# Optimization experiments

Hardware: AMD Instinct MI355X
Metric: run time of the kernel (lower is better)

Reference implementation:

```python
import jax, jax.numpy as jnp
import numpy as np
import math

B, L, H, E, D = 4, 2048, 8, 64, 64
EPS = 1e-6

def _adjust(x):
    # signed power-law (sqrt) then L2-normalize over feature dim
    y = jnp.sign(x) * jnp.sqrt(jnp.abs(x) + EPS)
    return y / (jnp.linalg.norm(y, axis=-1, keepdims=True) + EPS)

def setup_inputs() -> dict:
    key = jax.random.key(0)
    kq, kk, kv, ka = jax.random.split(key, 4)
    queries = jax.random.normal(kq, (B, L, H, E), dtype=jnp.float32)
    keys = jax.random.normal(kk, (B, L, H, E), dtype=jnp.float32)
    values = jax.random.normal(kv, (B, L, H, D), dtype=jnp.float32)
    # TriangularCausalMask: True above the diagonal => masked
    attn_mask = jnp.triu(jnp.ones((1, 1, L, L), dtype=bool), k=1)
    alpha = jax.random.normal(ka, (1,), dtype=jnp.float32) * 0.01
    return {"queries": queries, "keys": keys, "values": values,
            "attn_mask": attn_mask, "alpha": alpha}

def reference(queries, keys, values, attn_mask, alpha):
    Bq, Lq, Hq, Eq = queries.shape
    scale = 1.0 / math.sqrt(Eq)
    # Closed form of torch.autograd.functional.jacobian of
    # sum(einsum('blhe,bshe->bhls', q, k)):
    #   d/dq[b,l,h,e] = sum_s k[b,s,h,e]   (independent of l)
    #   d/dk[b,s,h,e] = sum_l q[b,l,h,e]   (independent of s)
    k_sum = jnp.sum(keys, axis=1, keepdims=True)      # [B,1,H,E]
    q_sum = jnp.sum(queries, axis=1, keepdims=True)   # [B,1,H,E]
    q_adj = _adjust(queries + alpha * k_sum)
    k_adj = _adjust(keys + alpha * q_sum)
    scores = jnp.einsum('blhe,bshe->bhls', q_adj, k_adj)  # [B,H,L,S]
    scores = jnp.where(attn_mask, -jnp.inf, scores)
    A = jax.nn.softmax(scale * scores, axis=-1)  # dropout inactive (eval)
    V = jnp.einsum('bhls,bshd->blhd', A, values)
    return V
```

## Files before the change

### kernel.cpp

```cpp
#include <hip/hip_runtime.h>
#include <hip/hip_bf16.h>
#include <math.h>

#define NB 4
#define NL 2048
#define NH 8
#define NE 64
#define ND 64
#define EPSF 1e-6f
#define CEXP 0.180336881f

typedef __attribute__((ext_vector_type(8))) short bf16x8;
typedef __attribute__((ext_vector_type(4))) float f32x4;

__global__ void sums_kernel(const float* __restrict__ q, const float* __restrict__ k,
                            float* __restrict__ qsum, float* __restrict__ ksum) {
  int bh = blockIdx.x;
  int lp = blockIdx.y;
  int e = threadIdx.x & 63, sub = threadIdx.x >> 6;
  int b = bh >> 3, h = bh & 7;
  size_t base = (((size_t)b * NL) * NH + h) * NE + e;
  const float* qp = q + base;
  const float* kp = k + base;
  float sq = 0.f, sk = 0.f;
#pragma unroll
  for (int i = 0; i < 16; ++i) {
    int l = lp * 64 + i * 4 + sub;
    size_t off = (size_t)l * NH * NE;
    sq += qp[off];
    sk += kp[off];
  }
  __shared__ float s1[256], s2[256];
  s1[threadIdx.x] = sq; s2[threadIdx.x] = sk;
  __syncthreads();
  if (sub == 0) {
    sq = s1[e] + s1[e + 64] + s1[e + 128] + s1[e + 192];
    sk = s2[e] + s2[e + 64] + s2[e + 128] + s2[e + 192];
    atomicAdd(&qsum[bh * NE + e], sq);
    atomicAdd(&ksum[bh * NE + e], sk);
  }
}

__global__ void adjust_kernel(const float* __restrict__ q, const float* __restrict__ k,
                              const float* __restrict__ qsum, const float* __restrict__ ksum,
                              const float* __restrict__ alpha,
                              __hip_bfloat16* __restrict__ qadj, __hip_bfloat16* __restrict__ kadj) {
  int wid = (int)((blockIdx.x * 256 + threadIdx.x) >> 6);
  int lane = threadIdx.x & 63;
  int h = wid & 7;
  int l = (wid >> 3) & (NL - 1);
  int b = wid >> 14;
  float al = alpha[0];
  size_t ioff = (((size_t)b * NL + l) * NH + h) * NE + lane;
  int bh = b * NH + h;
  float xq = q[ioff] + al * ksum[bh * NE + lane];
  float xk = k[ioff] + al * qsum[bh * NE + lane];
  float yq = (xq > 0.f) ? sqrtf(xq + EPSF) : ((xq < 0.f) ? -sqrtf(-xq + EPSF) : 0.f);
  float yk = (xk > 0.f) ? sqrtf(xk + EPSF) : ((xk < 0.f) ? -sqrtf(-xk + EPSF) : 0.f);
  float nq = yq * yq, nk = yk * yk;
#pragma unroll
  for (int m = 1; m < 64; m <<= 1) {
    nq += __shfl_xor(nq, m, 64);
    nk += __shfl_xor(nk, m, 64);
  }
  float rq = yq / (sqrtf(nq) + EPSF);
  float rk = yk / (sqrtf(nk) + EPSF);
  size_t ooff = ((size_t)bh * NL + l) * NE + lane;
  qadj[ooff] = __float2bfloat16(rq);
  kadj[ooff] = __float2bfloat16(rk);
}

__global__ void vtrans_kernel(const float* __restrict__ v, __hip_bfloat16* __restrict__ vt) {
  __shared__ __hip_bfloat16 tile[64][68];
  int s0 = blockIdx.x * 64;
  int bh = blockIdx.y;
  int b = bh >> 3, h = bh & 7;
  int t = threadIdx.x;
  {
    int sl = t >> 2, dg = t & 3;
    const float* src = v + (((size_t)b * NL + s0 + sl) * NH + h) * ND + dg * 16;
#pragma unroll
    for (int i = 0; i < 4; ++i) {
      float4 f = *(const float4*)(src + i * 4);
      tile[sl][dg * 16 + i * 4 + 0] = __float2bfloat16(f.x);
      tile[sl][dg * 16 + i * 4 + 1] = __float2bfloat16(f.y);
      tile[sl][dg * 16 + i * 4 + 2] = __float2bfloat16(f.z);
      tile[sl][dg * 16 + i * 4 + 3] = __float2bfloat16(f.w);
    }
  }
  __syncthreads();
  {
    int d = t >> 2, sg = t & 3;
    __align__(16) __hip_bfloat16 tmp[16];
#pragma unroll
    for (int i = 0; i < 16; ++i) tmp[i] = tile[sg * 16 + i][d];
    __hip_bfloat16* dst = vt + ((size_t)bh * ND + d) * NL + s0 + sg * 16;
    *(bf16x8*)(dst) = *(const bf16x8*)&tmp[0];
    *(bf16x8*)(dst + 8) = *(const bf16x8*)&tmp[8];
  }
}

__global__ __launch_bounds__(512) void attn_kernel(const __hip_bfloat16* __restrict__ qadj,
                                                   const __hip_bfloat16* __restrict__ kadj,
                                                   const __hip_bfloat16* __restrict__ vt,
                                                   float* __restrict__ out) {
  __shared__ __align__(16) char lds[49152];
  int bh = blockIdx.x;
  int pairid = blockIdx.y;
  int b = bh >> 3, h = bh & 7;
  int wave = threadIdx.x >> 6, lane = threadIdx.x & 63;
  int qr = lane & 15, eg = lane >> 4;
  char* ldsP = lds + 32768 + wave * 2048;
  const char* kgb = (const char*)(kadj + (size_t)bh * NL * NE);
  const char* vgb = (const char*)(vt + (size_t)bh * ND * NL);
  const char* qgb = (const char*)(qadj + (size_t)bh * NL * NE);

  auto STAGE = [&](int bufsel, int s0) {
    char* dstbase = lds + bufsel * 16384;
    if (wave < 4) {
#pragma unroll
      for (int c = 0; c < 2; ++c) {
        int T = wave * 2048 + c * 1024 + lane * 16;
        int S = T ^ (((T >> 7) & 7) << 4);
        __builtin_amdgcn_global_load_lds(
            (const __attribute__((address_space(1))) unsigned int*)(kgb + (size_t)s0 * 128 + S),
            (__attribute__((address_space(3))) unsigned int*)(dstbase + wave * 2048 + c * 1024),
            16, 0, 0);
      }
    } else {
      int w = wave - 4;
#pragma unroll
      for (int c = 0; c < 2; ++c) {
        int T = w * 2048 + c * 1024 + lane * 16;
        int S = T ^ (((T >> 7) & 7) << 4);
        int d = S >> 7, cc = S & 127;
        __builtin_amdgcn_global_load_lds(
            (const __attribute__((address_space(1))) unsigned int*)(vgb + ((size_t)d * NL + s0) * 2 + cc),
            (__attribute__((address_space(3))) unsigned int*)(dstbase + 8192 + w * 2048 + c * 1024),
            16, 0, 0);
      }
    }
  };

#pragma unroll 1
  for (int half = 0; half < 2; ++half) {
    int tile = (half == 0) ? pairid : (15 - pairid);
    int t0 = tile * 128;
    int nck = (t0 >> 6) + 2;
    int qw0 = t0 + wave * 16;

    bf16x8 qf0 = *(const bf16x8*)(qgb + ((size_t)(qw0 + qr) * NE + eg * 8) * 2);
    bf16x8 qf1 = *(const bf16x8*)(qgb + ((size_t)(qw0 + qr) * NE + 32 + eg * 8) * 2);

    f32x4 acc[4];
    float srun[4];
#pragma unroll
    for (int dc = 0; dc < 4; ++dc) acc[dc] = (f32x4){0.f, 0.f, 0.f, 0.f};
#pragma unroll
    for (int vv = 0; vv < 4; ++vv) srun[vv] = 0.f;

    STAGE(0, 0);
    asm volatile("s_waitcnt vmcnt(0)" ::: "memory");
    __builtin_amdgcn_sched_barrier(0);
    __builtin_amdgcn_s_barrier();

    int cur = 0;
#pragma unroll 1
    for (int ck = 0; ck < nck; ++ck) {
      int s0 = ck * 64;
      if (ck + 1 < nck) STAGE(cur ^ 1, s0 + 64);
      char* ldsK = lds + cur * 16384;
      char* ldsV = ldsK + 8192;

      float p[4][4];
#pragma unroll
      for (int st = 0; st < 4; ++st) {
        f32x4 a = (f32x4){0.f, 0.f, 0.f, 0.f};
        int row = st * 16 + qr;
        int swz = (row & 7) << 4;
        bf16x8 k0 = *(const bf16x8*)(ldsK + ((row * 128 + eg * 16) ^ swz));
        bf16x8 k1 = *(const bf16x8*)(ldsK + ((row * 128 + 64 + eg * 16) ^ swz));
        a = __builtin_amdgcn_mfma_f32_16x16x32_bf16(qf0, k0, a, 0, 0, 0);
        a = __builtin_amdgcn_mfma_f32_16x16x32_bf16(qf1, k1, a, 0, 0, 0);
#pragma unroll
        for (int vv = 0; vv < 4; ++vv) p[st][vv] = a[vv];
      }
      if (s0 + 63 > qw0) {
#pragma unroll
        for (int st = 0; st < 4; ++st)
#pragma unroll
          for (int vv = 0; vv < 4; ++vv)
            if (s0 + st * 16 + qr > qw0 + eg * 4 + vv) p[st][vv] = -1e30f;
      }
#pragma unroll
      for (int st = 0; st < 4; ++st)
#pragma unroll
        for (int vv = 0; vv < 4; ++vv) p[st][vv] = exp2f((p[st][vv] - 1.0f) * CEXP);
#pragma unroll
      for (int vv = 0; vv < 4; ++vv)
        srun[vv] += (p[0][vv] + p[1][vv]) + (p[2][vv] + p[3][vv]);

#pragma unroll
      for (int st = 0; st < 4; ++st)
#pragma unroll
        for (int vv = 0; vv < 4; ++vv) {
          int qrow = eg * 4 + vv, scol = st * 16 + qr;
          int byt = (qrow * 128 + scol * 2) ^ ((qrow & 7) << 4);
          *(__hip_bfloat16*)(ldsP + byt) = __float2bfloat16(p[st][vv]);
        }
      asm volatile("s_waitcnt lgkmcnt(0)" ::: "memory");
      __builtin_amdgcn_sched_barrier(0);

#pragma unroll
      for (int hh = 0; hh < 2; ++hh) {
        int pswz = (qr & 7) << 4;
        bf16x8 pa = *(const bf16x8*)(ldsP + ((qr * 128 + hh * 64 + eg * 16) ^ pswz));
#pragma unroll
        for (int dc = 0; dc < 4; ++dc) {
          int d = dc * 16 + qr;
          bf16x8 vf = *(const bf16x8*)(ldsV + ((d * 128 + hh * 64 + eg * 16) ^ ((d & 7) << 4)));
          acc[dc] = __builtin_amdgcn_mfma_f32_16x16x32_bf16(pa, vf, acc[dc], 0, 0, 0);
        }
      }

      asm volatile("s_waitcnt vmcnt(0)" ::: "memory");
      __builtin_amdgcn_sched_barrier(0);
      __builtin_amdgcn_s_barrier();
      cur ^= 1;
    }

#pragma unroll
    for (int vv = 0; vv < 4; ++vv) {
      float s = srun[vv];
#pragma unroll
      for (int m = 1; m < 16; m <<= 1) s += __shfl_xor(s, m, 16);
      float inv = 1.f / s;
      int l = qw0 + eg * 4 + vv;
      float* orow = out + (((size_t)b * NL + l) * NH + h) * ND;
#pragma unroll
      for (int dc = 0; dc < 4; ++dc) orow[dc * 16 + qr] = acc[dc][vv] * inv;
    }
  }
}

extern "C" void kernel_launch(void* const* d_in, const int* in_sizes, int n_in,
                              void* d_out, int out_size, void* d_ws, size_t ws_size,
                              hipStream_t stream) {
  const float* q = (const float*)d_in[0];
  const float* k = (const float*)d_in[1];
  const float* v = (const float*)d_in[2];
  const float* alpha = (const float*)d_in[4];
  float* out = (float*)d_out;
  char* ws = (char*)d_ws;

  __hip_bfloat16* qadj = (__hip_bfloat16*)(ws);
  __hip_bfloat16* kadj = (__hip_bfloat16*)(ws + 8388608);
  __hip_bfloat16* vt   = (__hip_bfloat16*)(ws + 16777216);
  float* qsum = (float*)(ws + 25165824);
  float* ksum = (float*)(ws + 25165824 + 8192);

  hipMemsetAsync(ws + 25165824, 0, 16384, stream);
  sums_kernel<<<dim3(32, 32), 256, 0, stream>>>(q, k, qsum, ksum);
  adjust_kernel<<<dim3(16384), 256, 0, stream>>>(q, k, qsum, ksum, alpha, qadj, kadj);
  vtrans_kernel<<<dim3(32, 32), 256, 0, stream>>>(v, vt);
  attn_kernel<<<dim3(32, 8), 512, 0, stream>>>(qadj, kadj, vt, out);
}
```

Before: 174.7 us.

## Fuse prep kernels, drop atomics, keep P in registers, triple-buffer attention

Replaces the atomic-based column sums with per-block partial sums that the consumer reduces, which also removes the memset. The adjust and V-transpose kernels are merged into one prep kernel using vectorized float4 loads, and V is stored in a permuted column order. The attention kernel now computes S^T so P stays in registers and feeds the PV MFMA directly without an LDS round trip. It also switches to 64-row tiles with 256 threads, a 3-stage load pipeline with partial vmcnt waits, and vectorized output stores. The risks are extra launch-level coupling between the stages and a fragile V permutation and pk indexing that must match the MFMA layout exactly.

New measurement: 162.8 us. 1.07x faster.

```diff
diff --git a/kernel.cpp b/kernel.cpp
--- a/kernel.cpp
+++ b/kernel.cpp
@@ -11,96 +11,150 @@
 #define CEXP 0.180336881f
 
 typedef __attribute__((ext_vector_type(8))) short bf16x8;
+typedef __attribute__((ext_vector_type(4))) short s16x4;
 typedef __attribute__((ext_vector_type(4))) float f32x4;
 
+static __device__ __forceinline__ unsigned short bfbits(float x) {
+  union { __hip_bfloat16 h; unsigned short u; } c;
+  c.h = __float2bfloat16(x);
+  return c.u;
+}
+static __device__ __forceinline__ float sgnsqrt(float x) {
+  return x > 0.f ? sqrtf(x + EPSF) : (x < 0.f ? -sqrtf(-x + EPSF) : 0.f);
+}
+
 __global__ void sums_kernel(const float* __restrict__ q, const float* __restrict__ k,
-                            float* __restrict__ qsum, float* __restrict__ ksum) {
-  int bh = blockIdx.x;
-  int lp = blockIdx.y;
-  int e = threadIdx.x & 63, sub = threadIdx.x >> 6;
-  int b = bh >> 3, h = bh & 7;
-  size_t base = (((size_t)b * NL) * NH + h) * NE + e;
-  const float* qp = q + base;
-  const float* kp = k + base;
-  float sq = 0.f, sk = 0.f;
-#pragma unroll
-  for (int i = 0; i < 16; ++i) {
-    int l = lp * 64 + i * 4 + sub;
-    size_t off = (size_t)l * NH * NE;
-    sq += qp[off];
-    sk += kp[off];
-  }
-  __shared__ float s1[256], s2[256];
-  s1[threadIdx.x] = sq; s2[threadIdx.x] = sk;
-  __syncthreads();
-  if (sub == 0) {
-    sq = s1[e] + s1[e + 64] + s1[e + 128] + s1[e + 192];
-    sk = s2[e] + s2[e + 64] + s2[e + 128] + s2[e + 192];
-    atomicAdd(&qsum[bh * NE + e], sq);
-    atomicAdd(&ksum[bh * NE + e], sk);
-  }
-}
-
-__global__ void adjust_kernel(const float* __restrict__ q, const float* __restrict__ k,
-                              const float* __restrict__ qsum, const float* __restrict__ ksum,
-                              const float* __restrict__ alpha,
-                              __hip_bfloat16* __restrict__ qadj, __hip_bfloat16* __restrict__ kadj) {
-  int wid = (int)((blockIdx.x * 256 + threadIdx.x) >> 6);
-  int lane = threadIdx.x & 63;
-  int h = wid & 7;
-  int l = (wid >> 3) & (NL - 1);
-  int b = wid >> 14;
-  float al = alpha[0];
-  size_t ioff = (((size_t)b * NL + l) * NH + h) * NE + lane;
-  int bh = b * NH + h;
-  float xq = q[ioff] + al * ksum[bh * NE + lane];
-  float xk = k[ioff] + al * qsum[bh * NE + lane];
-  float yq = (xq > 0.f) ? sqrtf(xq + EPSF) : ((xq < 0.f) ? -sqrtf(-xq + EPSF) : 0.f);
-  float yk = (xk > 0.f) ? sqrtf(xk + EPSF) : ((xk < 0.f) ? -sqrtf(-xk + EPSF) : 0.f);
-  float nq = yq * yq, nk = yk * yk;
-#pragma unroll
-  for (int m = 1; m < 64; m <<= 1) {
-    nq += __shfl_xor(nq, m, 64);
-    nk += __shfl_xor(nk, m, 64);
-  }
-  float rq = yq / (sqrtf(nq) + EPSF);
-  float rk = yk / (sqrtf(nk) + EPSF);
-  size_t ooff = ((size_t)bh * NL + l) * NE + lane;
-  qadj[ooff] = __float2bfloat16(rq);
-  kadj[ooff] = __float2bfloat16(rk);
-}
-
-__global__ void vtrans_kernel(const float* __restrict__ v, __hip_bfloat16* __restrict__ vt) {
-  __shared__ __hip_bfloat16 tile[64][68];
-  int s0 = blockIdx.x * 64;
-  int bh = blockIdx.y;
+                            float* __restrict__ pq, float* __restrict__ pk) {
+  int bh = blockIdx.x, lp = blockIdx.y;
   int b = bh >> 3, h = bh & 7;
   int t = threadIdx.x;
-  {
-    int sl = t >> 2, dg = t & 3;
-    const float* src = v + (((size_t)b * NL + s0 + sl) * NH + h) * ND + dg * 16;
-#pragma unroll
-    for (int i = 0; i < 4; ++i) {
-      float4 f = *(const float4*)(src + i * 4);
-      tile[sl][dg * 16 + i * 4 + 0] = __float2bfloat16(f.x);
-      tile[sl][dg * 16 + i * 4 + 1] = __float2bfloat16(f.y);
-      tile[sl][dg * 16 + i * 4 + 2] = __float2bfloat16(f.z);
-      tile[sl][dg * 16 + i * 4 + 3] = __float2bfloat16(f.w);
-    }
-  }
+  int eq = t & 15, lr = t >> 4;
+  int wave = t >> 6, lane = t & 63;
+  const float* qp = q + (((size_t)b * NL) * NH + h) * NE + eq * 4;
+  const float* kp = k + (((size_t)b * NL) * NH + h) * NE + eq * 4;
+  f32x4 aq = {0.f, 0.f, 0.f, 0.f}, ak = {0.f, 0.f, 0.f, 0.f};
+#pragma unroll
+  for (int i = 0; i < 8; ++i) {
+    int l = lp * 128 + i * 16 + lr;
+    size_t off = (size_t)l * NH * NE;
+    aq += *(const f32x4*)(qp + off);
+    ak += *(const f32x4*)(kp + off);
+  }
+#pragma unroll
+  for (int c = 0; c < 4; ++c) {
+    aq[c] += __shfl_xor(aq[c], 16, 64); aq[c] += __shfl_xor(aq[c], 32, 64);
+    ak[c] += __shfl_xor(ak[c], 16, 64); ak[c] += __shfl_xor(ak[c], 32, 64);
+  }
+  __shared__ f32x4 sq[4][16], sk[4][16];
+  if (lane < 16) { sq[wave][lane] = aq; sk[wave][lane] = ak; }
   __syncthreads();
-  {
-    int d = t >> 2, sg = t & 3;
-    __align__(16) __hip_bfloat16 tmp[16];
-#pragma unroll
-    for (int i = 0; i < 16; ++i) tmp[i] = tile[sg * 16 + i][d];
-    __hip_bfloat16* dst = vt + ((size_t)bh * ND + d) * NL + s0 + sg * 16;
-    *(bf16x8*)(dst) = *(const bf16x8*)&tmp[0];
-    *(bf16x8*)(dst + 8) = *(const bf16x8*)&tmp[8];
-  }
-}
-
-__global__ __launch_bounds__(512) void attn_kernel(const __hip_bfloat16* __restrict__ qadj,
+  if (t < 16) {
+    f32x4 s = sq[0][t] + sq[1][t] + sq[2][t] + sq[3][t];
+    *(f32x4*)(pq + ((size_t)bh * 16 + lp) * 64 + t * 4) = s;
+  } else if (t < 32) {
+    int e = t - 16;
+    f32x4 s = sk[0][e] + sk[1][e] + sk[2][e] + sk[3][e];
+    *(f32x4*)(pk + ((size_t)bh * 16 + e < 0 ? 0 : ((size_t)bh * 16) + 0) * 0 + ((size_t)bh * 16 + lp) * 64 + e * 4) = s;
+  }
+}
+
+__global__ void prep_kernel(const float* __restrict__ q, const float* __restrict__ k,
+                            const float* __restrict__ v,
+                            const float* __restrict__ pq, const float* __restrict__ pk,
+                            const float* __restrict__ alpha,
+                            __hip_bfloat16* __restrict__ qadj, __hip_bfloat16* __restrict__ kadj,
+                            __hip_bfloat16* __restrict__ vt) {
+  __shared__ float aqs[8][68], aks[8][68];
+  __shared__ __hip_bfloat16 tile[64][68];
+  int t = threadIdx.x;
+  if (blockIdx.x < 1024) {
+    int rid0 = blockIdx.x * 64;
+    int b = rid0 >> 14;
+    {
+      int h = t >> 5, j = t & 31;
+      const float* pqp = pq + ((size_t)(b * 8 + h) * 16) * 64 + j * 2;
+      const float* pkp = pk + ((size_t)(b * 8 + h) * 16) * 64 + j * 2;
+      float s0 = 0.f, s1 = 0.f, u0 = 0.f, u1 = 0.f;
+#pragma unroll
+      for (int lp = 0; lp < 16; ++lp) {
+        s0 += pqp[lp * 64]; s1 += pqp[lp * 64 + 1];
+        u0 += pkp[lp * 64]; u1 += pkp[lp * 64 + 1];
+      }
+      float al = alpha[0];
+      aqs[h][j * 2] = al * s0; aqs[h][j * 2 + 1] = al * s1;
+      aks[h][j * 2] = al * u0; aks[h][j * 2 + 1] = al * u1;
+    }
+    __syncthreads();
+    int eq = t & 15, lr = t >> 4;
+#pragma unroll
+    for (int p = 0; p < 4; ++p) {
+      int rid = rid0 + p * 16 + lr;
+      int h = rid & 7, l = (rid >> 3) & 2047;
+      f32x4 q4 = *(const f32x4*)(q + (size_t)rid * 64 + eq * 4);
+      f32x4 k4 = *(const f32x4*)(k + (size_t)rid * 64 + eq * 4);
+      f32x4 xq = q4 + *(const f32x4*)&aks[h][eq * 4];
+      f32x4 xk = k4 + *(const f32x4*)&aqs[h][eq * 4];
+      float yq[4], yk[4];
+      float nq = 0.f, nk = 0.f;
+#pragma unroll
+      for (int c = 0; c < 4; ++c) {
+        yq[c] = sgnsqrt(xq[c]); nq += yq[c] * yq[c];
+        yk[c] = sgnsqrt(xk[c]); nk += yk[c] * yk[c];
+      }
+#pragma unroll
+      for (int m = 1; m < 16; m <<= 1) {
+        nq += __shfl_xor(nq, m, 16);
+        nk += __shfl_xor(nk, m, 16);
+      }
+      float iq = 1.f / (sqrtf(nq) + EPSF);
+      float ik = 1.f / (sqrtf(nk) + EPSF);
+      s16x4 uq, uk;
+#pragma unroll
+      for (int c = 0; c < 4; ++c) {
+        uq[c] = (short)bfbits(yq[c] * iq);
+        uk[c] = (short)bfbits(yk[c] * ik);
+      }
+      size_t ooff = ((size_t)(b * 8 + h) * 2048 + l) * 64 + eq * 4;
+      *(s16x4*)((char*)qadj + ooff * 2) = uq;
+      *(s16x4*)((char*)kadj + ooff * 2) = uk;
+    }
+  } else {
+    int blk = blockIdx.x - 1024;
+    int s0 = (blk & 31) * 64;
+    int bh = blk >> 5;
+    int b = bh >> 3, h = bh & 7;
+    {
+      int sl = t >> 2, dg = t & 3;
+      const float* src = v + (((size_t)b * NL + s0 + sl) * NH + h) * ND + dg * 16;
+#pragma unroll
+      for (int i = 0; i < 4; ++i) {
+        f32x4 f = *(const f32x4*)(src + i * 4);
+        tile[sl][dg * 16 + i * 4 + 0] = __float2bfloat16(f[0]);
+        tile[sl][dg * 16 + i * 4 + 1] = __float2bfloat16(f[1]);
+        tile[sl][dg * 16 + i * 4 + 2] = __float2bfloat16(f[2]);
+        tile[sl][dg * 16 + i * 4 + 3] = __float2bfloat16(f[3]);
+      }
+    }
+    __syncthreads();
+    {
+      int d = t >> 2, sg = t & 3;
+      __align__(16) __hip_bfloat16 tmp[16];
+#pragma unroll
+      for (int i = 0; i < 16; ++i) {
+        int c = sg * 16 + i;
+        int blk32 = c >> 5, cc = c & 31;
+        int cq = cc >> 2, ege = cq >> 1, hi = cq & 1;
+        int s_local = blk32 * 32 + hi * 16 + ege * 4 + (cc & 3);
+        tmp[i] = tile[s_local][d];
+      }
+      __hip_bfloat16* dst = vt + ((size_t)bh * ND + d) * NL + s0 + sg * 16;
+      *(bf16x8*)(dst) = *(const bf16x8*)&tmp[0];
+      *(bf16x8*)(dst + 8) = *(const bf16x8*)&tmp[8];
+    }
+  }
+}
+
+__global__ __launch_bounds__(256) void attn_kernel(const __hip_bfloat16* __restrict__ qadj,
                                                    const __hip_bfloat16* __restrict__ kadj,
                                                    const __hip_bfloat16* __restrict__ vt,
                                                    float* __restrict__ out) {
@@ -110,66 +164,65 @@
   int b = bh >> 3, h = bh & 7;
   int wave = threadIdx.x >> 6, lane = threadIdx.x & 63;
   int qr = lane & 15, eg = lane >> 4;
-  char* ldsP = lds + 32768 + wave * 2048;
   const char* kgb = (const char*)(kadj + (size_t)bh * NL * NE);
   const char* vgb = (const char*)(vt + (size_t)bh * ND * NL);
   const char* qgb = (const char*)(qadj + (size_t)bh * NL * NE);
 
-  auto STAGE = [&](int bufsel, int s0) {
+  auto STAGE = [&](int bufsel, int ck) {
     char* dstbase = lds + bufsel * 16384;
-    if (wave < 4) {
-#pragma unroll
-      for (int c = 0; c < 2; ++c) {
-        int T = wave * 2048 + c * 1024 + lane * 16;
+    int s0 = ck * 64;
+#pragma unroll
+    for (int c = 0; c < 4; ++c) {
+      int T = (wave * 4 + c) * 1024 + lane * 16;
+      const char* src;
+      if (T < 8192) {
         int S = T ^ (((T >> 7) & 7) << 4);
-        __builtin_amdgcn_global_load_lds(
-            (const __attribute__((address_space(1))) unsigned int*)(kgb + (size_t)s0 * 128 + S),
-            (__attribute__((address_space(3))) unsigned int*)(dstbase + wave * 2048 + c * 1024),
-            16, 0, 0);
-      }
-    } else {
-      int w = wave - 4;
-#pragma unroll
-      for (int c = 0; c < 2; ++c) {
-        int T = w * 2048 + c * 1024 + lane * 16;
-        int S = T ^ (((T >> 7) & 7) << 4);
+        src = kgb + (size_t)s0 * 128 + S;
+      } else {
+        int T2 = T - 8192;
+        int S = T2 ^ (((T2 >> 7) & 7) << 4);
         int d = S >> 7, cc = S & 127;
-        __builtin_amdgcn_global_load_lds(
-            (const __attribute__((address_space(1))) unsigned int*)(vgb + ((size_t)d * NL + s0) * 2 + cc),
-            (__attribute__((address_space(3))) unsigned int*)(dstbase + 8192 + w * 2048 + c * 1024),
-            16, 0, 0);
-      }
+        src = vgb + ((size_t)d * NL + s0) * 2 + cc;
+      }
+      __builtin_amdgcn_global_load_lds(
+          (const __attribute__((address_space(1))) unsigned int*)src,
+          (__attribute__((address_space(3))) unsigned int*)(dstbase + (wave * 4 + c) * 1024),
+          16, 0, 0);
     }
   };
 
 #pragma unroll 1
   for (int half = 0; half < 2; ++half) {
-    int tile = (half == 0) ? pairid : (15 - pairid);
-    int t0 = tile * 128;
-    int nck = (t0 >> 6) + 2;
+    int tile = half ? (31 - pairid) : pairid;
+    int t0 = tile * 64;
+    int nck = tile + 1;
     int qw0 = t0 + wave * 16;
 
-    bf16x8 qf0 = *(const bf16x8*)(qgb + ((size_t)(qw0 + qr) * NE + eg * 8) * 2);
-    bf16x8 qf1 = *(const bf16x8*)(qgb + ((size_t)(qw0 + qr) * NE + 32 + eg * 8) * 2);
+    bf16x8 qf0 = *(const bf16x8*)(qgb + (size_t)(qw0 + qr) * 128 + eg * 16);
+    bf16x8 qf1 = *(const bf16x8*)(qgb + (size_t)(qw0 + qr) * 128 + 64 + eg * 16);
 
     f32x4 acc[4];
-    float srun[4];
 #pragma unroll
     for (int dc = 0; dc < 4; ++dc) acc[dc] = (f32x4){0.f, 0.f, 0.f, 0.f};
-#pragma unroll
-    for (int vv = 0; vv < 4; ++vv) srun[vv] = 0.f;
-
+    float srun = 0.f;
+
+    if (half) {
+      asm volatile("s_waitcnt vmcnt(0)" ::: "memory");
+      __builtin_amdgcn_sched_barrier(0);
+      __builtin_amdgcn_s_barrier();
+    }
     STAGE(0, 0);
-    asm volatile("s_waitcnt vmcnt(0)" ::: "memory");
-    __builtin_amdgcn_sched_barrier(0);
-    __builtin_amdgcn_s_barrier();
-
-    int cur = 0;
+    if (nck > 1) STAGE(1, 1);
+
 #pragma unroll 1
     for (int ck = 0; ck < nck; ++ck) {
-      int s0 = ck * 64;
-      if (ck + 1 < nck) STAGE(cur ^ 1, s0 + 64);
-      char* ldsK = lds + cur * 16384;
+      if (ck + 1 < nck) asm volatile("s_waitcnt vmcnt(4)" ::: "memory");
+      else              asm volatile("s_waitcnt vmcnt(0)" ::: "memory");
+      __builtin_amdgcn_sched_barrier(0);
+      __builtin_amdgcn_s_barrier();
+      __builtin_amdgcn_sched_barrier(0);
+      if (ck + 2 < nck) STAGE((ck + 2) % 3, ck + 2);
+      char* ldsK = lds + (ck % 3) * 16384;
       char* ldsV = ldsK + 8192;
 
       float p[4][4];
@@ -180,66 +233,49 @@
         int swz = (row & 7) << 4;
         bf16x8 k0 = *(const bf16x8*)(ldsK + ((row * 128 + eg * 16) ^ swz));
         bf16x8 k1 = *(const bf16x8*)(ldsK + ((row * 128 + 64 + eg * 16) ^ swz));
-        a = __builtin_amdgcn_mfma_f32_16x16x32_bf16(qf0, k0, a, 0, 0, 0);
-        a = __builtin_amdgcn_mfma_f32_16x16x32_bf16(qf1, k1, a, 0, 0, 0);
-#pragma unroll
-        for (int vv = 0; vv < 4; ++vv) p[st][vv] = a[vv];
-      }
-      if (s0 + 63 > qw0) {
+        a = __builtin_amdgcn_mfma_f32_16x16x32_bf16(k0, qf0, a, 0, 0, 0);
+        a = __builtin_amdgcn_mfma_f32_16x16x32_bf16(k1, qf1, a, 0, 0, 0);
+#pragma unroll
+        for (int r = 0; r < 4; ++r) p[st][r] = a[r];
+      }
+      if (ck == nck - 1) {
 #pragma unroll
         for (int st = 0; st < 4; ++st)
 #pragma unroll
-          for (int vv = 0; vv < 4; ++vv)
-            if (s0 + st * 16 + qr > qw0 + eg * 4 + vv) p[st][vv] = -1e30f;
+          for (int r = 0; r < 4; ++r)
+            if (t0 + st * 16 + eg * 4 + r > qw0 + qr) p[st][r] = -1e30f;
       }
 #pragma unroll
       for (int st = 0; st < 4; ++st)
 #pragma unroll
-        for (int vv = 0; vv < 4; ++vv) p[st][vv] = exp2f((p[st][vv] - 1.0f) * CEXP);
-#pragma unroll
-      for (int vv = 0; vv < 4; ++vv)
-        srun[vv] += (p[0][vv] + p[1][vv]) + (p[2][vv] + p[3][vv]);
-
-#pragma unroll
-      for (int st = 0; st < 4; ++st)
-#pragma unroll
-        for (int vv = 0; vv < 4; ++vv) {
-          int qrow = eg * 4 + vv, scol = st * 16 + qr;
-          int byt = (qrow * 128 + scol * 2) ^ ((qrow & 7) << 4);
-          *(__hip_bfloat16*)(ldsP + byt) = __float2bfloat16(p[st][vv]);
+        for (int r = 0; r < 4; ++r) p[st][r] = exp2f((p[st][r] - 1.0f) * CEXP);
+      srun += ((p[0][0] + p[0][1] + p[0][2] + p[0][3]) + (p[1][0] + p[1][1] + p[1][2] + p[1][3])) +
+              ((p[2][0] + p[2][1] + p[2][2] + p[2][3]) + (p[3][0] + p[3][1] + p[3][2] + p[3][3]));
+
+#pragma unroll
+      for (int pp = 0; pp < 2; ++pp) {
+        bf16x8 pb;
+#pragma unroll
+        for (int j = 0; j < 4; ++j) {
+          pb[j] = (short)bfbits(p[2 * pp][j]);
+          pb[4 + j] = (short)bfbits(p[2 * pp + 1][j]);
         }
-      asm volatile("s_waitcnt lgkmcnt(0)" ::: "memory");
-      __builtin_amdgcn_sched_barrier(0);
-
-#pragma unroll
-      for (int hh = 0; hh < 2; ++hh) {
-        int pswz = (qr & 7) << 4;
-        bf16x8 pa = *(const bf16x8*)(ldsP + ((qr * 128 + hh * 64 + eg * 16) ^ pswz));
 #pragma unroll
         for (int dc = 0; dc < 4; ++dc) {
           int d = dc * 16 + qr;
-          bf16x8 vf = *(const bf16x8*)(ldsV + ((d * 128 + hh * 64 + eg * 16) ^ ((d & 7) << 4)));
-          acc[dc] = __builtin_amdgcn_mfma_f32_16x16x32_bf16(pa, vf, acc[dc], 0, 0, 0);
+          bf16x8 vf = *(const bf16x8*)(ldsV + ((d * 128 + pp * 64 + eg * 16) ^ ((d & 7) << 4)));
+          acc[dc] = __builtin_amdgcn_mfma_f32_16x16x32_bf16(vf, pb, acc[dc], 0, 0, 0);
         }
       }
-
-      asm volatile("s_waitcnt vmcnt(0)" ::: "memory");
-      __builtin_amdgcn_sched_barrier(0);
-      __builtin_amdgcn_s_barrier();
-      cur ^= 1;
-    }
-
-#pragma unroll
-    for (int vv = 0; vv < 4; ++vv) {
-      float s = srun[vv];
-#pragma unroll
-      for (int m = 1; m < 16; m <<= 1) s += __shfl_xor(s, m, 16);
-      float inv = 1.f / s;
-      int l = qw0 + eg * 4 + vv;
-      float* orow = out + (((size_t)b * NL + l) * NH + h) * ND;
-#pragma unroll
-      for (int dc = 0; dc < 4; ++dc) orow[dc * 16 + qr] = acc[dc][vv] * inv;
-    }
+    }
+
+    srun += __shfl_xor(srun, 16, 64);
+    srun += __shfl_xor(srun, 32, 64);
+    float inv = 1.f / srun;
+    int l = qw0 + qr;
+    float* orow = out + (((size_t)b * NL + l) * NH + h) * ND;
+#pragma unroll
+    for (int dc = 0; dc < 4; ++dc) *(f32x4*)(orow + dc * 16 + eg * 4) = acc[dc] * inv;
   }
 }
 
@@ -256,12 +292,10 @@
   __hip_bfloat16* qadj = (__hip_bfloat16*)(ws);
   __hip_bfloat16* kadj = (__hip_bfloat16*)(ws + 8388608);
   __hip_bfloat16* vt   = (__hip_bfloat16*)(ws + 16777216);
-  float* qsum = (float*)(ws + 25165824);
-  float* ksum = (float*)(ws + 25165824 + 8192);
-
-  hipMemsetAsync(ws + 25165824, 0, 16384, stream);
-  sums_kernel<<<dim3(32, 32), 256, 0, stream>>>(q, k, qsum, ksum);
-  adjust_kernel<<<dim3(16384), 256, 0, stream>>>(q, k, qsum, ksum, alpha, qadj, kadj);
-  vtrans_kernel<<<dim3(32, 32), 256, 0, stream>>>(v, vt);
-  attn_kernel<<<dim3(32, 8), 512, 0, stream>>>(qadj, kadj, vt, out);
-}
+  float* pq = (float*)(ws + 25165824);
+  float* pk = (float*)(ws + 25165824 + 131072);
+
+  sums_kernel<<<dim3(32, 16), 256, 0, stream>>>(q, k, pq, pk);
+  prep_kernel<<<dim3(2048), 256, 0, stream>>>(q, k, v, pq, pk, alpha, qadj, kadj, vt);
+  attn_kernel<<<dim3(32, 16), 256, 0, stream>>>(qadj, kadj, vt, out);
+}
```
